# Kernel optimization log

Measured on AMD Instinct MI355X. Metric: run time of the kernel, lower is better.

Reference implementation:

```python
import jax, jax.numpy as jnp
import numpy as np

N_ROWS, N_COLS = 4, 4
EPS = 1e-5


def setup_inputs() -> dict:
    key = jax.random.key(0)
    ks = jax.random.split(key, 4)
    x = jax.random.normal(ks[0], (32, 32, 256, 256), dtype=jnp.float32)
    gamma = jnp.ones((32,), dtype=jnp.float32)
    beta = jnp.zeros((32,), dtype=jnp.float32)
    prelu_a = jnp.full((1,), 0.25, dtype=jnp.float32)  # torch PReLU default init
    conv_w = jax.random.normal(ks[1], (32, 32, 3, 3), dtype=jnp.float32) * (1.0 / np.sqrt(32 * 9))
    conv_b = jax.random.normal(ks[2], (32,), dtype=jnp.float32) * 0.01
    return {"x": x, "gamma": gamma, "beta": beta, "prelu_a": prelu_a,
            "conv_w": conv_w, "conv_b": conv_b}


def reference(x, gamma, beta, prelu_a, conv_w, conv_b):
    B, C, H, W = x.shape
    rh, rw = H // N_ROWS, W // N_COLS
    # Fold the region grid into a leading region axis: [R, B, C, rh, rw]
    xr = x.reshape(B, C, N_ROWS, rh, N_COLS, rw)
    xr = xr.transpose(2, 4, 0, 1, 3, 5).reshape(N_ROWS * N_COLS, B, C, rh, rw)
    # BatchNorm (training mode): per-region, per-channel stats over (B, rh, rw)
    mean = xr.mean(axis=(1, 3, 4), keepdims=True)
    var = jnp.mean((xr - mean) ** 2, axis=(1, 3, 4), keepdims=True)  # biased var
    g = gamma[None, None, :, None, None]
    b = beta[None, None, :, None, None]
    y = (xr - mean) * jax.lax.rsqrt(var + EPS) * g + b
    # PReLU with a single shared slope
    y = jnp.where(y > 0, y, prelu_a[0] * y)
    # Conv2d 3x3 pad=1 applied per region (zero padding at region borders)
    yb = y.reshape(N_ROWS * N_COLS * B, C, rh, rw)
    out = jax.lax.conv_general_dilated(
        yb, conv_w, window_strides=(1, 1), padding=((1, 1), (1, 1)),
        dimension_numbers=("NCHW", "OIHW", "NCHW"))
    out = out + conv_b[None, :, None, None]
    # Reassemble region grid -> full image
    out = out.reshape(N_ROWS, N_COLS, B, C, rh, rw)
    out = out.transpose(2, 3, 0, 4, 1, 5).reshape(B, C, H, W)
    return out
```

## Files before the change

### kernel.cpp

```cpp
#include <hip/hip_runtime.h>
#include <hip/hip_bf16.h>


#define EPS 1e-5f

typedef float f32x4 __attribute__((ext_vector_type(4)));
typedef __bf16 bf16x8 __attribute__((ext_vector_type(8)));
typedef short short8 __attribute__((ext_vector_type(8)));

__device__ inline short f2bf(float f) {
  union { __hip_bfloat16 h; short s; } u;
  u.h = __float2bfloat16(f);
  return u.s;
}

__global__ __launch_bounds__(256) void stats_partial(
    const float* __restrict__ x, float* __restrict__ ws_sum,
    float* __restrict__ ws_sq) {
  int plane = blockIdx.x;
  const float* base = x + (size_t)plane * 65536;
  int t = threadIdx.x;
  float s[4] = {0.f, 0.f, 0.f, 0.f}, q[4] = {0.f, 0.f, 0.f, 0.f};
#pragma unroll
  for (int R = 0; R < 4; ++R) {
#pragma unroll
    for (int ii = 0; ii < 16; ++ii) {
      int idx4 = (R * 16 + ii) * 256 + t;
      float4 v = *reinterpret_cast<const float4*>(base + (size_t)idx4 * 4);
      s[R] += (v.x + v.y) + (v.z + v.w);
      q[R] += (v.x * v.x + v.y * v.y) + (v.z * v.z + v.w * v.w);
    }
  }
#pragma unroll
  for (int R = 0; R < 4; ++R) {
#pragma unroll
    for (int off = 8; off; off >>= 1) {
      s[R] += __shfl_down(s[R], off);
      q[R] += __shfl_down(q[R], off);
    }
  }
  __shared__ float red[2][4][4][4];
  int lane = t & 63, wv = t >> 6;
  if ((lane & 15) == 0) {
    int Cc = lane >> 4;
#pragma unroll
    for (int R = 0; R < 4; ++R) {
      red[0][wv][Cc][R] = s[R];
      red[1][wv][Cc][R] = q[R];
    }
  }
  __syncthreads();
  if (t < 16) {
    int R = t >> 2, Cc = t & 3;
    float S = 0.f, Q = 0.f;
#pragma unroll
    for (int w = 0; w < 4; ++w) {
      S += red[0][w][Cc][R];
      Q += red[1][w][Cc][R];
    }
    ws_sum[plane * 16 + t] = S;
    ws_sq[plane * 16 + t] = Q;
  }
}

__global__ __launch_bounds__(256) void weights_prep(
    const float* __restrict__ conv_w, unsigned short* __restrict__ wfrag) {
  int idx = blockIdx.x * 256 + threadIdx.x;
  if (idx >= 18 * 64) return;
  int lane = idx & 63;
  int th = idx >> 6;
  int t = th >> 1, h = th & 1;
  int dy = t / 3, dx = t - dy * 3;
  int oc = h * 16 + (lane & 15);
  int ic0 = (lane >> 4) * 8;
#pragma unroll
  for (int j = 0; j < 8; ++j) {
    float w = conv_w[((oc * 32 + ic0 + j) * 3 + dy) * 3 + dx];
    wfrag[(size_t)idx * 8 + j] = (unsigned short)f2bf(w);
  }
}

__global__ __launch_bounds__(256) void conv_mfma(
    const float* __restrict__ x, const unsigned short* __restrict__ wfrag,
    const float* __restrict__ conv_b, const float* __restrict__ prelu_a,
    const float* __restrict__ ws_sum, const float* __restrict__ ws_sq,
    const float* __restrict__ gamma, const float* __restrict__ beta,
    float* __restrict__ out) {
  __shared__ short lds_y[10 * 64 * 32];

  int blk0 = blockIdx.x;
  int blk = (blk0 & 7) * 512 + (blk0 >> 3);
  int rt = blk & 7;
  int p = (blk >> 3) & 15;
  int b = blk >> 7;
  int R = p >> 2, Cc = p & 3;
  int h0 = rt * 8;
  int tid = threadIdx.x;
  int lane = tid & 63;
  float pa = prelu_a[0];

  float* abuf = (float*)lds_y;
  if (tid < 32) {
    int c = tid;
    float S = 0.f, Q = 0.f;
#pragma unroll
    for (int bb = 0; bb < 32; ++bb) {
      int idx = (bb * 32 + c) * 16 + p;
      S += ws_sum[idx];
      Q += ws_sq[idx];
    }
    const float inv = 1.0f / 131072.0f;
    float mean = S * inv;
    float var = Q * inv - mean * mean;
    float rstd = rsqrtf(var + EPS);
    float a = rstd * gamma[c];
    abuf[c] = a;
    abuf[32 + c] = beta[c] - mean * a;
  }
  __syncthreads();

  int s = (tid >> 4) & 3;
  int c4 = tid & 15;
  int srb = tid >> 6;
  int ic0 = s * 8;

  float a_r[8], b_r[8];
#pragma unroll
  for (int j = 0; j < 8; ++j) {
    a_r[j] = abuf[ic0 + j];
    b_r[j] = abuf[32 + ic0 + j];
  }
  __syncthreads();

  auto stage_load = [&](f32x4(&vv)[8], int sr) {
    int lr = h0 - 1 + sr;
#pragma unroll
    for (int kk = 0; kk < 8; ++kk) vv[kk] = f32x4{0.f, 0.f, 0.f, 0.f};
    if ((unsigned)lr < 64u) {
      const float* xp =
          x + (((size_t)(b * 32 + ic0) * 256 + R * 64 + lr) * 256) + Cc * 64 +
          c4 * 4;
#pragma unroll
      for (int kk = 0; kk < 8; ++kk)
        vv[kk] = *reinterpret_cast<const f32x4*>(xp + (size_t)kk * 65536);
    }
  };
  auto stage_write = [&](const f32x4(&vv)[8], int sr) {
#pragma unroll
    for (int j = 0; j < 4; ++j) {
      short8 pk;
#pragma unroll
      for (int kk = 0; kk < 8; ++kk) {
        float e = fmaf(a_r[kk], vv[kk][j], b_r[kk]);
        e = e > 0.f ? e : pa * e;
        pk[kk] = f2bf(e);
      }
      int col = c4 * 4 + j;
      int slot = (s + (col >> 1)) & 3;
      *reinterpret_cast<short8*>(&lds_y[(sr * 64 + col) * 32 + slot * 8]) = pk;
    }
  };

  {
    f32x4 va[8], vb[8], vc[8];
    stage_load(va, srb);
    stage_load(vb, srb + 4);
    stage_write(va, srb);
    if (tid < 128) stage_load(vc, srb + 8);
    stage_write(vb, srb + 4);
    if (tid < 128) stage_write(vc, srb + 8);
  }
  __syncthreads();

  bf16x8 wf[18];
#pragma unroll
  for (int th = 0; th < 18; ++th) {
    short8 sv =
        *reinterpret_cast<const short8*>(wfrag + ((size_t)th * 64 + lane) * 8);
    wf[th] = __builtin_bit_cast(bf16x8, sv);
  }
  int l15 = lane & 15, l4 = lane >> 4;
  f32x4 bias0, bias1;
#pragma unroll
  for (int i = 0; i < 4; ++i) {
    bias0[i] = conv_b[l4 * 4 + i];
    bias1[i] = conv_b[16 + l4 * 4 + i];
  }

  int wv = tid >> 6;
  const short8 z8 = {0, 0, 0, 0, 0, 0, 0, 0};
  for (int g = 0; g < 8; ++g) {
    int gi = wv * 8 + g;
    int r = gi >> 2;
    int c0 = (gi & 3) * 16;
    f32x4 acc0 = bias0, acc1 = bias1;
#pragma unroll
    for (int t9 = 0; t9 < 9; ++t9) {
      const int dy = t9 / 3, dx = t9 - dy * 3;
      int sr = r + dy;
      int col_in = c0 + l15 + dx - 1;
      int colc = col_in & 63;
      int slot = (l4 + (colc >> 1)) & 3;
      short8 sv = *reinterpret_cast<const short8*>(
          &lds_y[(sr * 64 + colc) * 32 + slot * 8]);
      if (dx == 0) {
        if (c0 == 0 && l15 == 0) sv = z8;
      }
      if (dx == 2) {
        if (c0 == 48 && l15 == 15) sv = z8;
      }
      bf16x8 bv = __builtin_bit_cast(bf16x8, sv);
      acc0 = __builtin_amdgcn_mfma_f32_16x16x32_bf16(wf[t9 * 2], bv, acc0, 0, 0, 0);
      acc1 = __builtin_amdgcn_mfma_f32_16x16x32_bf16(wf[t9 * 2 + 1], bv, acc1, 0, 0, 0);
    }
    int grow = R * 64 + h0 + r;
    int gcol = Cc * 64 + c0 + l15;
    float* ob = out + (size_t)b * 2097152 + (size_t)grow * 256 + gcol;
#pragma unroll
    for (int i = 0; i < 4; ++i) {
      ob[(size_t)(l4 * 4 + i) * 65536] = acc0[i];
      ob[(size_t)(16 + l4 * 4 + i) * 65536] = acc1[i];
    }
  }
}

extern "C" void kernel_launch(void* const* d_in, const int* in_sizes, int n_in,
                              void* d_out, int out_size, void* d_ws,
                              size_t ws_size, hipStream_t stream) {
  const float* x = (const float*)d_in[0];
  const float* gamma = (const float*)d_in[1];
  const float* beta = (const float*)d_in[2];
  const float* prelu_a = (const float*)d_in[3];
  const float* conv_w = (const float*)d_in[4];
  const float* conv_b = (const float*)d_in[5];
  float* out = (float*)d_out;

  float* ws = (float*)d_ws;
  float* ws_sum = ws;
  float* ws_sq = ws + 16384;
  unsigned short* wfrag = (unsigned short*)(ws + 32768);

  weights_prep<<<5, 256, 0, stream>>>(conv_w, wfrag);
  stats_partial<<<1024, 256, 0, stream>>>(x, ws_sum, ws_sq);
  conv_mfma<<<4096, 256, 0, stream>>>(x, wfrag, conv_b, prelu_a, ws_sum, ws_sq,
                                      gamma, beta, out);
}
```

Before: 190.1 us.

## Split normalization into separate bf16 pass and DMA-load it into conv LDS

```diff
diff --git a/kernel.cpp b/kernel.cpp
--- a/kernel.cpp
+++ b/kernel.cpp
@@ -12,6 +12,12 @@
   union { __hip_bfloat16 h; short s; } u;
   u.h = __float2bfloat16(f);
   return u.s;
+}
+
+__device__ inline void dma16(const void* g, void* l) {
+  __builtin_amdgcn_global_load_lds(
+      (const __attribute__((address_space(1))) unsigned int*)g,
+      (__attribute__((address_space(3))) unsigned int*)l, 16, 0, 0);
 }
 
 __global__ __launch_bounds__(256) void stats_partial(
@@ -80,12 +86,82 @@
   }
 }
 
-__global__ __launch_bounds__(256) void conv_mfma(
-    const float* __restrict__ x, const unsigned short* __restrict__ wfrag,
-    const float* __restrict__ conv_b, const float* __restrict__ prelu_a,
-    const float* __restrict__ ws_sum, const float* __restrict__ ws_sq,
-    const float* __restrict__ gamma, const float* __restrict__ beta,
-    float* __restrict__ out) {
+__global__ __launch_bounds__(256) void norm_write(
+    const float* __restrict__ x, const float* __restrict__ ws_sum,
+    const float* __restrict__ ws_sq, const float* __restrict__ gamma,
+    const float* __restrict__ beta, const float* __restrict__ prelu_a,
+    unsigned short* __restrict__ y) {
+  __shared__ float abuf[64];
+  int blk = blockIdx.x;
+  int qr = blk & 3;
+  int p = (blk >> 2) & 15;
+  int b = 31 - (blk >> 6);
+  int R = p >> 2, Cc = p & 3;
+  int tid = threadIdx.x;
+
+  if (tid < 32) {
+    int c = tid;
+    float S = 0.f, Q = 0.f;
+#pragma unroll
+    for (int bb = 0; bb < 32; ++bb) {
+      int idx = (bb * 32 + c) * 16 + p;
+      S += ws_sum[idx];
+      Q += ws_sq[idx];
+    }
+    const float inv = 1.0f / 131072.0f;
+    float mean = S * inv;
+    float var = Q * inv - mean * mean;
+    float rstd = rsqrtf(var + EPS);
+    float a = rstd * gamma[c];
+    abuf[c] = a;
+    abuf[32 + c] = beta[c] - mean * a;
+  }
+  __syncthreads();
+
+  int s = tid & 3;
+  int c4 = (tid >> 2) & 15;
+  int rsub = tid >> 6;
+  int ic0 = s * 8;
+  float a_r[8], b_r[8];
+#pragma unroll
+  for (int j = 0; j < 8; ++j) {
+    a_r[j] = abuf[ic0 + j];
+    b_r[j] = abuf[32 + ic0 + j];
+  }
+  float pa = prelu_a[0];
+
+  unsigned short* yp = y + ((size_t)(b * 16 + p)) * 131072;
+  const float* xb =
+      x + ((size_t)(b * 32) * 65536) + (size_t)R * 64 * 256 + Cc * 64;
+
+  for (int it = 0; it < 4; ++it) {
+    int row = qr * 16 + it * 4 + rsub;
+    const float* xr = xb + (size_t)ic0 * 65536 + row * 256 + c4 * 4;
+    f32x4 v[8];
+#pragma unroll
+    for (int kk = 0; kk < 8; ++kk)
+      v[kk] = *reinterpret_cast<const f32x4*>(xr + (size_t)kk * 65536);
+#pragma unroll
+    for (int j = 0; j < 4; ++j) {
+      short8 pk;
+#pragma unroll
+      for (int kk = 0; kk < 8; ++kk) {
+        float e = fmaf(a_r[kk], v[kk][j], b_r[kk]);
+        e = e > 0.f ? e : pa * e;
+        pk[kk] = f2bf(e);
+      }
+      int col = c4 * 4 + j;
+      int slot = (s + (col >> 1)) & 3;
+      *reinterpret_cast<short8*>(&yp[((size_t)row * 64 + col) * 32 + slot * 8]) =
+          pk;
+    }
+  }
+}
+
+__global__ __launch_bounds__(256) void conv_dma(
+    const unsigned short* __restrict__ y,
+    const unsigned short* __restrict__ wfrag,
+    const float* __restrict__ conv_b, float* __restrict__ out) {
   __shared__ short lds_y[10 * 64 * 32];
 
   int blk0 = blockIdx.x;
@@ -97,80 +173,7 @@
   int h0 = rt * 8;
   int tid = threadIdx.x;
   int lane = tid & 63;
-  float pa = prelu_a[0];
-
-  float* abuf = (float*)lds_y;
-  if (tid < 32) {
-    int c = tid;
-    float S = 0.f, Q = 0.f;
-#pragma unroll
-    for (int bb = 0; bb < 32; ++bb) {
-      int idx = (bb * 32 + c) * 16 + p;
-      S += ws_sum[idx];
-      Q += ws_sq[idx];
-    }
-    const float inv = 1.0f / 131072.0f;
-    float mean = S * inv;
-    float var = Q * inv - mean * mean;
-    float rstd = rsqrtf(var + EPS);
-    float a = rstd * gamma[c];
-    abuf[c] = a;
-    abuf[32 + c] = beta[c] - mean * a;
-  }
-  __syncthreads();
-
-  int s = (tid >> 4) & 3;
-  int c4 = tid & 15;
-  int srb = tid >> 6;
-  int ic0 = s * 8;
-
-  float a_r[8], b_r[8];
-#pragma unroll
-  for (int j = 0; j < 8; ++j) {
-    a_r[j] = abuf[ic0 + j];
-    b_r[j] = abuf[32 + ic0 + j];
-  }
-  __syncthreads();
-
-  auto stage_load = [&](f32x4(&vv)[8], int sr) {
-    int lr = h0 - 1 + sr;
-#pragma unroll
-    for (int kk = 0; kk < 8; ++kk) vv[kk] = f32x4{0.f, 0.f, 0.f, 0.f};
-    if ((unsigned)lr < 64u) {
-      const float* xp =
-          x + (((size_t)(b * 32 + ic0) * 256 + R * 64 + lr) * 256) + Cc * 64 +
-          c4 * 4;
-#pragma unroll
-      for (int kk = 0; kk < 8; ++kk)
-        vv[kk] = *reinterpret_cast<const f32x4*>(xp + (size_t)kk * 65536);
-    }
-  };
-  auto stage_write = [&](const f32x4(&vv)[8], int sr) {
-#pragma unroll
-    for (int j = 0; j < 4; ++j) {
-      short8 pk;
-#pragma unroll
-      for (int kk = 0; kk < 8; ++kk) {
-        float e = fmaf(a_r[kk], vv[kk][j], b_r[kk]);
-        e = e > 0.f ? e : pa * e;
-        pk[kk] = f2bf(e);
-      }
-      int col = c4 * 4 + j;
-      int slot = (s + (col >> 1)) & 3;
-      *reinterpret_cast<short8*>(&lds_y[(sr * 64 + col) * 32 + slot * 8]) = pk;
-    }
-  };
-
-  {
-    f32x4 va[8], vb[8], vc[8];
-    stage_load(va, srb);
-    stage_load(vb, srb + 4);
-    stage_write(va, srb);
-    if (tid < 128) stage_load(vc, srb + 8);
-    stage_write(vb, srb + 4);
-    if (tid < 128) stage_write(vc, srb + 8);
-  }
-  __syncthreads();
+  int wv = tid >> 6;
 
   bf16x8 wf[18];
 #pragma unroll
@@ -187,8 +190,24 @@
     bias1[i] = conv_b[16 + l4 * 4 + i];
   }
 
-  int wv = tid >> 6;
+  const unsigned short* yp = y + ((size_t)(b * 16 + p)) * 131072;
   const short8 z8 = {0, 0, 0, 0, 0, 0, 0, 0};
+#pragma unroll
+  for (int k = 0; k < 10; ++k) {
+    int i = wv * 10 + k;
+    int row = i >> 2, q = i & 3;
+    int lr = h0 - 1 + row;
+    short* ldst = &lds_y[row * 2048 + q * 512];
+    if ((unsigned)lr < 64u) {
+      const unsigned short* g =
+          yp + (size_t)lr * 2048 + q * 512 + (size_t)lane * 8;
+      dma16(g, ldst);
+    } else {
+      *reinterpret_cast<short8*>(&lds_y[row * 2048 + q * 512 + lane * 8]) = z8;
+    }
+  }
+  __syncthreads();
+
   for (int g = 0; g < 8; ++g) {
     int gi = wv * 8 + g;
     int r = gi >> 2;
@@ -239,9 +258,11 @@
   float* ws_sum = ws;
   float* ws_sq = ws + 16384;
   unsigned short* wfrag = (unsigned short*)(ws + 32768);
+  unsigned short* y = (unsigned short*)(ws + 40960);
 
   weights_prep<<<5, 256, 0, stream>>>(conv_w, wfrag);
   stats_partial<<<1024, 256, 0, stream>>>(x, ws_sum, ws_sq);
-  conv_mfma<<<4096, 256, 0, stream>>>(x, wfrag, conv_b, prelu_a, ws_sum, ws_sq,
-                                      gamma, beta, out);
-}
+  norm_write<<<2048, 256, 0, stream>>>(x, ws_sum, ws_sq, gamma, beta, prelu_a,
+                                       y);
+  conv_dma<<<4096, 256, 0, stream>>>(y, wfrag, conv_b, out);
+}
```

New measurement: 256.4 us. 1.35x slower.

## Warp-specialize conv kernel into producer/consumer waves with double-buffered LDS tiles

Applied to the files above, without the earlier changes.

```diff
diff --git a/kernel.cpp b/kernel.cpp
--- a/kernel.cpp
+++ b/kernel.cpp
@@ -80,26 +80,26 @@
   }
 }
 
-__global__ __launch_bounds__(256) void conv_mfma(
+__global__ __launch_bounds__(512) void conv_ws(
     const float* __restrict__ x, const unsigned short* __restrict__ wfrag,
     const float* __restrict__ conv_b, const float* __restrict__ prelu_a,
     const float* __restrict__ ws_sum, const float* __restrict__ ws_sq,
     const float* __restrict__ gamma, const float* __restrict__ beta,
     float* __restrict__ out) {
-  __shared__ short lds_y[10 * 64 * 32];
+  __shared__ short buf2[2][10 * 64 * 32];
+  __shared__ float abuf[64];
 
   int blk0 = blockIdx.x;
-  int blk = (blk0 & 7) * 512 + (blk0 >> 3);
-  int rt = blk & 7;
-  int p = (blk >> 3) & 15;
-  int b = blk >> 7;
+  int blk = (blk0 & 7) * 64 + (blk0 >> 3);
+  int p = blk & 15;
+  int b = blk >> 4;
   int R = p >> 2, Cc = p & 3;
-  int h0 = rt * 8;
   int tid = threadIdx.x;
   int lane = tid & 63;
+  bool producer = tid >= 256;
+  int t0 = tid & 255;
   float pa = prelu_a[0];
 
-  float* abuf = (float*)lds_y;
   if (tid < 32) {
     int c = tid;
     float S = 0.f, Q = 0.f;
@@ -119,20 +119,18 @@
   }
   __syncthreads();
 
-  int s = (tid >> 4) & 3;
-  int c4 = tid & 15;
-  int srb = tid >> 6;
+  int s = (t0 >> 4) & 3;
+  int c4 = t0 & 15;
+  int srb = t0 >> 6;
   int ic0 = s * 8;
-
   float a_r[8], b_r[8];
 #pragma unroll
   for (int j = 0; j < 8; ++j) {
     a_r[j] = abuf[ic0 + j];
     b_r[j] = abuf[32 + ic0 + j];
   }
-  __syncthreads();
-
-  auto stage_load = [&](f32x4(&vv)[8], int sr) {
+
+  auto stage_load = [&](f32x4(&vv)[8], int sr, int h0) {
     int lr = h0 - 1 + sr;
 #pragma unroll
     for (int kk = 0; kk < 8; ++kk) vv[kk] = f32x4{0.f, 0.f, 0.f, 0.f};
@@ -145,7 +143,7 @@
         vv[kk] = *reinterpret_cast<const f32x4*>(xp + (size_t)kk * 65536);
     }
   };
-  auto stage_write = [&](const f32x4(&vv)[8], int sr) {
+  auto stage_write = [&](short* buf, const f32x4(&vv)[8], int sr) {
 #pragma unroll
     for (int j = 0; j < 4; ++j) {
       short8 pk;
@@ -157,70 +155,84 @@
       }
       int col = c4 * 4 + j;
       int slot = (s + (col >> 1)) & 3;
-      *reinterpret_cast<short8*>(&lds_y[(sr * 64 + col) * 32 + slot * 8]) = pk;
-    }
-  };
-
-  {
+      *reinterpret_cast<short8*>(&buf[(sr * 64 + col) * 32 + slot * 8]) = pk;
+    }
+  };
+  auto stage_tile = [&](short* buf, int t) {
+    int h0 = t * 8;
     f32x4 va[8], vb[8], vc[8];
-    stage_load(va, srb);
-    stage_load(vb, srb + 4);
-    stage_write(va, srb);
-    if (tid < 128) stage_load(vc, srb + 8);
-    stage_write(vb, srb + 4);
-    if (tid < 128) stage_write(vc, srb + 8);
-  }
+    stage_load(va, srb, h0);
+    stage_load(vb, srb + 4, h0);
+    stage_write(buf, va, srb);
+    if (t0 < 128) stage_load(vc, srb + 8, h0);
+    stage_write(buf, vb, srb + 4);
+    if (t0 < 128) stage_write(buf, vc, srb + 8);
+  };
+
+  int l15 = lane & 15, l4 = lane >> 4;
+  int wv = t0 >> 6;
+  bf16x8 wf[18];
+  f32x4 bias0, bias1;
+  if (!producer) {
+#pragma unroll
+    for (int th = 0; th < 18; ++th) {
+      short8 sv = *reinterpret_cast<const short8*>(
+          wfrag + ((size_t)th * 64 + lane) * 8);
+      wf[th] = __builtin_bit_cast(bf16x8, sv);
+    }
+#pragma unroll
+    for (int i = 0; i < 4; ++i) {
+      bias0[i] = conv_b[l4 * 4 + i];
+      bias1[i] = conv_b[16 + l4 * 4 + i];
+    }
+  }
+  const short8 z8 = {0, 0, 0, 0, 0, 0, 0, 0};
+
+  auto compute_tile = [&](const short* buf, int t) {
+    int h0 = t * 8;
+    for (int g = 0; g < 8; ++g) {
+      int gi = wv * 8 + g;
+      int r = gi >> 2;
+      int c0 = (gi & 3) * 16;
+      f32x4 acc0 = bias0, acc1 = bias1;
+#pragma unroll
+      for (int t9 = 0; t9 < 9; ++t9) {
+        const int dy = t9 / 3, dx = t9 - dy * 3;
+        int sr = r + dy;
+        int col_in = c0 + l15 + dx - 1;
+        int colc = col_in & 63;
+        int slot = (l4 + (colc >> 1)) & 3;
+        short8 sv = *reinterpret_cast<const short8*>(
+            &buf[(sr * 64 + colc) * 32 + slot * 8]);
+        if (dx == 0 && c0 == 0 && l15 == 0) sv = z8;
+        if (dx == 2 && c0 == 48 && l15 == 15) sv = z8;
+        bf16x8 bv = __builtin_bit_cast(bf16x8, sv);
+        acc0 = __builtin_amdgcn_mfma_f32_16x16x32_bf16(wf[t9 * 2], bv, acc0,
+                                                       0, 0, 0);
+        acc1 = __builtin_amdgcn_mfma_f32_16x16x32_bf16(wf[t9 * 2 + 1], bv,
+                                                       acc1, 0, 0, 0);
+      }
+      int grow = R * 64 + h0 + r;
+      int gcol = Cc * 64 + c0 + l15;
+      float* ob = out + (size_t)b * 2097152 + (size_t)grow * 256 + gcol;
+#pragma unroll
+      for (int i = 0; i < 4; ++i) {
+        ob[(size_t)(l4 * 4 + i) * 65536] = acc0[i];
+        ob[(size_t)(16 + l4 * 4 + i) * 65536] = acc1[i];
+      }
+    }
+  };
+
+  if (producer) stage_tile(buf2[0], 0);
   __syncthreads();
 
-  bf16x8 wf[18];
-#pragma unroll
-  for (int th = 0; th < 18; ++th) {
-    short8 sv =
-        *reinterpret_cast<const short8*>(wfrag + ((size_t)th * 64 + lane) * 8);
-    wf[th] = __builtin_bit_cast(bf16x8, sv);
-  }
-  int l15 = lane & 15, l4 = lane >> 4;
-  f32x4 bias0, bias1;
-#pragma unroll
-  for (int i = 0; i < 4; ++i) {
-    bias0[i] = conv_b[l4 * 4 + i];
-    bias1[i] = conv_b[16 + l4 * 4 + i];
-  }
-
-  int wv = tid >> 6;
-  const short8 z8 = {0, 0, 0, 0, 0, 0, 0, 0};
-  for (int g = 0; g < 8; ++g) {
-    int gi = wv * 8 + g;
-    int r = gi >> 2;
-    int c0 = (gi & 3) * 16;
-    f32x4 acc0 = bias0, acc1 = bias1;
-#pragma unroll
-    for (int t9 = 0; t9 < 9; ++t9) {
-      const int dy = t9 / 3, dx = t9 - dy * 3;
-      int sr = r + dy;
-      int col_in = c0 + l15 + dx - 1;
-      int colc = col_in & 63;
-      int slot = (l4 + (colc >> 1)) & 3;
-      short8 sv = *reinterpret_cast<const short8*>(
-          &lds_y[(sr * 64 + colc) * 32 + slot * 8]);
-      if (dx == 0) {
-        if (c0 == 0 && l15 == 0) sv = z8;
-      }
-      if (dx == 2) {
-        if (c0 == 48 && l15 == 15) sv = z8;
-      }
-      bf16x8 bv = __builtin_bit_cast(bf16x8, sv);
-      acc0 = __builtin_amdgcn_mfma_f32_16x16x32_bf16(wf[t9 * 2], bv, acc0, 0, 0, 0);
-      acc1 = __builtin_amdgcn_mfma_f32_16x16x32_bf16(wf[t9 * 2 + 1], bv, acc1, 0, 0, 0);
-    }
-    int grow = R * 64 + h0 + r;
-    int gcol = Cc * 64 + c0 + l15;
-    float* ob = out + (size_t)b * 2097152 + (size_t)grow * 256 + gcol;
-#pragma unroll
-    for (int i = 0; i < 4; ++i) {
-      ob[(size_t)(l4 * 4 + i) * 65536] = acc0[i];
-      ob[(size_t)(16 + l4 * 4 + i) * 65536] = acc1[i];
-    }
+  for (int t = 0; t < 8; ++t) {
+    if (producer) {
+      if (t < 7) stage_tile(buf2[(t + 1) & 1], t + 1);
+    } else {
+      compute_tile(buf2[t & 1], t);
+    }
+    __syncthreads();
   }
 }
 
@@ -242,6 +254,6 @@
 
   weights_prep<<<5, 256, 0, stream>>>(conv_w, wfrag);
   stats_partial<<<1024, 256, 0, stream>>>(x, ws_sum, ws_sq);
-  conv_mfma<<<4096, 256, 0, stream>>>(x, wfrag, conv_b, prelu_a, ws_sum, ws_sq,
-                                      gamma, beta, out);
-}
+  conv_ws<<<512, 512, 0, stream>>>(x, wfrag, conv_b, prelu_a, ws_sum, ws_sq,
+                                   gamma, beta, out);
+}
```

After: 190.1 us. About the same (-0.0%).
